# Optimization experiments

Hardware: AMD Instinct MI355X
Metric: run time of the kernel (lower is better)

Reference implementation:

```python
import jax, jax.numpy as jnp
import numpy as np

B, N, D = 4, 512, 256  # batch, num_diseases, feature_dim == hidden_dim
H = 256                # hidden_dim
EPS = 1e-5

def _layernorm(x, g, b):
    m = jnp.mean(x, axis=-1, keepdims=True)
    v = jnp.mean((x - m) ** 2, axis=-1, keepdims=True)
    return (x - m) * jax.lax.rsqrt(v + EPS) * g + b

def setup_inputs() -> dict:
    key = jax.random.key(0)
    ks = jax.random.split(key, 16)
    s = 0.02
    return {
        "x": jax.random.normal(ks[0], (B, N, D), jnp.float32),
        "area_matrix": jax.random.uniform(ks[1], (B, N), jnp.float32),
        "co_occurrence": jax.random.uniform(ks[2], (N, N), jnp.float32),
        "Wq": jax.random.normal(ks[3], (H, D), jnp.float32) * s,
        "bq": jnp.zeros((H,), jnp.float32),
        "Wk": jax.random.normal(ks[4], (H, D), jnp.float32) * s,
        "bk": jnp.zeros((H,), jnp.float32),
        "Wv": jax.random.normal(ks[5], (H, D), jnp.float32) * s,
        "bv": jnp.zeros((H,), jnp.float32),
        "We1": jax.random.normal(ks[6], (H, 2), jnp.float32) * 0.5,
        "be1": jnp.zeros((H,), jnp.float32),
        "We2": jax.random.normal(ks[7], (1, H), jnp.float32) * s,
        "be2": jnp.zeros((1,), jnp.float32),
        "Wo": jax.random.normal(ks[8], (H, H), jnp.float32) * s,
        "bo": jnp.zeros((H,), jnp.float32),
        "g_ot": jnp.ones((H,), jnp.float32),
        "b_ot": jnp.zeros((H,), jnp.float32),
        "g1": jnp.ones((H,), jnp.float32),
        "b1": jnp.zeros((H,), jnp.float32),
        "g2": jnp.ones((H,), jnp.float32),
        "b2": jnp.zeros((H,), jnp.float32),
    }

def reference(x, area_matrix, co_occurrence, Wq, bq, Wk, bk, Wv, bv,
              We1, be1, We2, be2, Wo, bo, g_ot, b_ot, g1, b1, g2, b2):
    # projections: (B, N, H)
    q = jnp.einsum('bnd,hd->bnh', x, Wq) + bq
    k = jnp.einsum('bnd,hd->bnh', x, Wk) + bk
    v = jnp.einsum('bnd,hd->bnh', x, Wv) + bv
    attn_scores = jnp.einsum('bih,bjh->bij', q, k) / jnp.sqrt(jnp.float32(H))
    # edge inputs: (B, N, N, 2) = stack(broadcast area along last N, broadcast co-occ along batch)
    area = jnp.broadcast_to(area_matrix[:, :, None], (B, N, N))
    co = jnp.broadcast_to(co_occurrence[None], (B, N, N))
    edge_inputs = jnp.stack([area, co], axis=-1)
    h = jax.nn.relu(jnp.einsum('bije,he->bijh', edge_inputs, We1) + be1)
    edge_weights = jax.nn.sigmoid(jnp.einsum('bijh,oh->bijo', h, We2) + be2)[..., 0]
    attn_probs = jax.nn.softmax(attn_scores * edge_weights, axis=-1)  # dropout = identity (eval)
    out = jnp.einsum('bij,bjh->bih', attn_probs, v)
    out = _layernorm(out, g1, b1)
    out = jax.nn.relu(_layernorm(jnp.einsum('bnh,oh->bno', out, Wo) + bo, g_ot, b_ot))
    out = _layernorm(out + x, g2, b2)
    return out
```

## Files before the change

### kernel.cpp

```cpp
#include <hip/hip_runtime.h>

typedef unsigned short u16;
typedef unsigned int u32;

#define NB 4
#define NN 512
#define ND 256
#define NH 256
#define TI 4

typedef __attribute__((ext_vector_type(8))) short short8;
typedef __attribute__((ext_vector_type(4))) float f32x4;

__device__ __forceinline__ u16 bfq(float f) {
    u32 t; __builtin_memcpy(&t, &f, 4);
    u32 r = (t + 0x7FFFu + ((t >> 16) & 1u)) >> 16;
    return (u16)r;
}

__device__ __forceinline__ short8 cvt8(float4 a, float4 b) {
    short8 r;
    r[0] = (short)bfq(a.x); r[1] = (short)bfq(a.y);
    r[2] = (short)bfq(a.z); r[3] = (short)bfq(a.w);
    r[4] = (short)bfq(b.x); r[5] = (short)bfq(b.y);
    r[6] = (short)bfq(b.z); r[7] = (short)bfq(b.w);
    return r;
}

__device__ __forceinline__ float waveReduceSum(float v) {
#pragma unroll
    for (int o = 32; o > 0; o >>= 1) v += __shfl_down(v, o);
    return v;
}

__device__ __forceinline__ void blockReduce8(float4& va, float4& vb, float4* red) {
#pragma unroll
    for (int o = 32; o > 0; o >>= 1) {
        va.x += __shfl_down(va.x, o); va.y += __shfl_down(va.y, o);
        va.z += __shfl_down(va.z, o); va.w += __shfl_down(va.w, o);
        vb.x += __shfl_down(vb.x, o); vb.y += __shfl_down(vb.y, o);
        vb.z += __shfl_down(vb.z, o); vb.w += __shfl_down(vb.w, o);
    }
    int wid = threadIdx.x >> 6;
    __syncthreads();
    if ((threadIdx.x & 63) == 0) { red[2 * wid] = va; red[2 * wid + 1] = vb; }
    __syncthreads();
    float4 ra = red[0], rb = red[1];
#pragma unroll
    for (int w = 1; w < 8; ++w) {
        float4 ua = red[2 * w], ub = red[2 * w + 1];
        ra.x += ua.x; ra.y += ua.y; ra.z += ua.z; ra.w += ua.w;
        rb.x += ub.x; rb.y += ub.y; rb.z += ub.z; rb.w += ub.w;
    }
    va = ra; vb = rb;
}

__global__ __launch_bounds__(256) void qkv_mfma(
    const float* __restrict__ x,
    const float* __restrict__ Wq, const float* __restrict__ bq,
    const float* __restrict__ Wk, const float* __restrict__ bk,
    const float* __restrict__ Wv, const float* __restrict__ bv,
    u16* __restrict__ qb, u16* __restrict__ kb, u16* __restrict__ vt)
{
    const int lane = threadIdx.x & 63, wave = threadIdx.x >> 6;
    const int r0 = blockIdx.x * 64 + wave * 16;
    const int out0 = blockIdx.y * 16;
    const int which = blockIdx.y >> 4;
    const float* W   = (which == 0) ? Wq : (which == 1) ? Wk : Wv;
    const float* bia = (which == 0) ? bq : (which == 1) ? bk : bv;

    const int m = lane & 15, koff = (lane >> 4) * 8;
    const float* Apf = x + (size_t)(r0 + m) * 256 + koff;
    const float* Bpf = W + (size_t)((out0 & 255) + m) * 256 + koff;

    f32x4 acc = {0.f, 0.f, 0.f, 0.f};
#pragma unroll
    for (int ks = 0; ks < 8; ++ks) {
        float4 a0 = *(const float4*)(Apf + ks * 32);
        float4 a1 = *(const float4*)(Apf + ks * 32 + 4);
        float4 b0 = *(const float4*)(Bpf + ks * 32);
        float4 b1 = *(const float4*)(Bpf + ks * 32 + 4);
        acc = __builtin_amdgcn_mfma_f32_16x16x32_bf16(cvt8(a0, a1), cvt8(b0, b1), acc, 0, 0, 0);
    }

    const int oc = (out0 + m) & 255;
    const float bias = bia[oc];
    const int rbase = r0 + (lane >> 4) * 4;
#pragma unroll
    for (int reg = 0; reg < 4; ++reg) {
        int R = rbase + reg;
        u16 val = bfq(acc[reg] + bias);
        if (which == 0)      qb[(size_t)R * 256 + oc] = val;
        else if (which == 1) kb[(size_t)R * 256 + oc] = val;
        else                 vt[((size_t)(R >> 9) * 256 + oc) * 512 + (R & 511)] = val;
    }
}

#define PSTR 520
#define YSTR 264
__global__ __launch_bounds__(512, 4) void fused_kernel(
    const float* __restrict__ x, const float* __restrict__ area, const float* __restrict__ co,
    const float* __restrict__ We1, const float* __restrict__ be1,
    const float* __restrict__ We2, const float* __restrict__ be2,
    const float* __restrict__ Wo, const float* __restrict__ bo,
    const float* __restrict__ g_ot, const float* __restrict__ b_ot,
    const float* __restrict__ g1, const float* __restrict__ b1,
    const float* __restrict__ g2, const float* __restrict__ b2,
    const u16* __restrict__ qb, const u16* __restrict__ kb,
    const u16* __restrict__ vt, float* __restrict__ out)
{
    const int tid = threadIdx.x;
    const int bsw = (blockIdx.x & 7) * 64 + (blockIdx.x >> 3);
    const int b = bsw >> 7;
    const int i0 = (bsw & 127) << 2;
    const int lane = tid & 63, w = tid >> 6;
    const int g = lane >> 4, c = lane & 15;
    const int hP = tid & 255, half = tid >> 8;

    __shared__ float histS[1024], histB[1024];
    __shared__ float pvbuf[1024];
    __shared__ u16 srow16[16 * PSTR];
    __shared__ u16 y16[16 * YSTR];
    __shared__ float4 red8b[16];
    __shared__ float sBaseS[4], sBaseB[4], redA[8], redB[8];

    const int m = lane & 15, koff = (lane >> 4) * 8;
    const u16* Ap    = qb + (size_t)(b * 512 + i0 + m) * 256 + koff;
    const u16* Kbase = kb + (size_t)(b * 512 + m) * 256 + koff;

    short8 afr[8];
#pragma unroll
    for (int ks = 0; ks < 8; ++ks) afr[ks] = *(const short8*)(Ap + ks * 32);

    float cov[4];
#pragma unroll
    for (int t = 0; t < 4; ++t)
        cov[t] = co[(size_t)(i0 + g) * NN + (w * 4 + t) * 16 + c];

    float xv[TI];
#pragma unroll
    for (int ti = 0; ti < TI; ++ti)
        xv[ti] = x[(size_t)(b * NN + i0 + ti) * ND + hP];

    const float bov  = bo[hP];
    const float g1v  = g1[hP],  b1v  = b1[hP];
    const float gotv = g_ot[hP], botv = b_ot[hP];
    const float g2v  = g2[hP],  b2v  = b2[hP];
    const float be2f = be2[0];

    histS[tid] = 0.f; histS[tid + 512] = 0.f;
    histB[tid] = 0.f; histB[tid + 512] = 0.f;
    {
        u32* s32 = (u32*)srow16;
        for (int i = tid; i < 4160; i += 512) s32[i] = 0u;
        u32* y32 = (u32*)y16;
        for (int i = tid; i < 2112; i += 512) y32[i] = 0u;
    }
    __syncthreads();

    {
        const int s = tid >> 7, h0 = tid & 127;
        const float a = area[b * NN + i0 + s];
        float baS = 0.f, baB = 0.f;
#pragma unroll
        for (int k = 0; k < 2; ++k) {
            const int h = h0 + 128 * k;
            const float w10 = We1[2 * h], w11 = We1[2 * h + 1];
            const float w2v = We2[h], be1v = be1[h];
            const float al = fmaf(a, w10, be1v);
            const float sl = w11 * w2v, bb = al * w2v;
            if (w11 == 0.f) {
                if (al > 0.f) baB += bb;
            } else {
                float tt = -al / w11;
                if (w11 > 0.f) {
                    if (tt <= 0.f)      { baS += sl; baB += bb; }
                    else if (tt < 1.f) {
                        int u = (int)(tt * 256.f); u = u > 255 ? 255 : u;
                        atomicAdd(&histS[s * 256 + u], sl);
                        atomicAdd(&histB[s * 256 + u], bb);
                    }
                } else {
                    if (tt >= 1.f)      { baS += sl; baB += bb; }
                    else if (tt > 0.f) {
                        baS += sl; baB += bb;
                        int u = (int)(tt * 256.f); u = u > 255 ? 255 : u;
                        atomicAdd(&histS[s * 256 + u], -sl);
                        atomicAdd(&histB[s * 256 + u], -bb);
                    }
                }
            }
        }
        float rS = waveReduceSum(baS), rB = waveReduceSum(baB);
        if (lane == 0) { redA[w] = rS; redB[w] = rB; }
    }

    f32x4 sacc[4];
    {
#pragma unroll
        for (int t = 0; t < 4; ++t) {
            const u16* Bp = Kbase + (size_t)(w * 4 + t) * 16 * 256;
            f32x4 acc = {0.f, 0.f, 0.f, 0.f};
#pragma unroll
            for (int ks = 0; ks < 8; ++ks) {
                short8 bb = *(const short8*)(Bp + ks * 32);
                acc = __builtin_amdgcn_mfma_f32_16x16x32_bf16(afr[ks], bb, acc, 0, 0, 0);
            }
            sacc[t] = acc;
        }
    }
    __syncthreads();
    if (tid < 4) {
        sBaseS[tid] = redA[2 * tid] + redA[2 * tid + 1];
        sBaseB[tid] = redB[2 * tid] + redB[2 * tid + 1];
    }

    {
        const int s = w & 3;
        float* hp = (w < 4) ? histS : histB;
        float b0 = hp[s * 256 + 4 * lane + 0];
        float b1 = hp[s * 256 + 4 * lane + 1];
        float b2 = hp[s * 256 + 4 * lane + 2];
        float b3 = hp[s * 256 + 4 * lane + 3];
        float p0 = b0, p1 = p0 + b1, p2 = p1 + b2, p3 = p2 + b3;
        float incl = p3;
#pragma unroll
        for (int off = 1; off < 64; off <<= 1) {
            float t = __shfl_up(incl, off);
            if (lane >= off) incl += t;
        }
        float excl = incl - p3;
        hp[s * 256 + 4 * lane + 0] = p0 + excl;
        hp[s * 256 + 4 * lane + 1] = p1 + excl;
        hp[s * 256 + 4 * lane + 2] = p2 + excl;
        hp[s * 256 + 4 * lane + 3] = p3 + excl;
    }
    __syncthreads();

    {
#pragma unroll
        for (int t = 0; t < 4; ++t) {
            const int j = (w * 4 + t) * 16 + c;
            float s0 = __shfl(sacc[t][0], c);
            float s1 = __shfl(sacc[t][1], c);
            float s2 = __shfl(sacc[t][2], c);
            float s3 = __shfl(sacc[t][3], c);
            float sv = (g == 0) ? s0 : (g == 1) ? s1 : (g == 2) ? s2 : s3;
            float cc = cov[t];
            int u = (int)(cc * 256.f); u = u > 255 ? 255 : u;
            float Sg = sBaseS[g] + histS[g * 256 + u];
            float Bg = sBaseB[g] + histB[g * 256 + u];
            float e = fmaf(cc, Sg, Bg) + be2f;
            float ew = 1.f / (1.f + __expf(-e));
            srow16[g * PSTR + j] = bfq(__expf(sv * 0.0625f * ew));
        }
    }
    __syncthreads();

    {
        const int t0 = 2 * w, t1 = 2 * w + 1;
        const u16* B0p = vt + ((size_t)(b * 256 + t0 * 16 + m)) * 512 + koff;
        const u16* B1p = vt + ((size_t)(b * 256 + t1 * 16 + m)) * 512 + koff;
        const u16* Arow = srow16 + m * PSTR + koff;
        f32x4 acc0 = {0.f, 0.f, 0.f, 0.f}, acc1 = {0.f, 0.f, 0.f, 0.f};
#pragma unroll
        for (int ks = 0; ks < 16; ++ks) {
            short8 a  = *(const short8*)(Arow + ks * 32);
            short8 b0 = *(const short8*)(B0p + ks * 32);
            short8 b1 = *(const short8*)(B1p + ks * 32);
            acc0 = __builtin_amdgcn_mfma_f32_16x16x32_bf16(a, b0, acc0, 0, 0, 0);
            acc1 = __builtin_amdgcn_mfma_f32_16x16x32_bf16(a, b1, acc1, 0, 0, 0);
        }
        if (lane < 16) {
#pragma unroll
            for (int reg = 0; reg < 4; ++reg) {
                pvbuf[reg * 256 + t0 * 16 + lane] = acc0[reg];
                pvbuf[reg * 256 + t1 * 16 + lane] = acc1[reg];
            }
        }
        __syncthreads();
    }

    float4 sa, sb;
    float accv[TI];
#pragma unroll
    for (int ti = 0; ti < TI; ++ti) {
        accv[ti] = (half == 0) ? pvbuf[ti * 256 + hP] : 0.f;
        ((float*)&sa)[ti] = accv[ti];
        ((float*)&sb)[ti] = accv[ti] * accv[ti];
    }
    blockReduce8(sa, sb, red8b);
    if (half == 0) {
#pragma unroll
        for (int ti = 0; ti < TI; ++ti) {
            float mean = ((const float*)&sa)[ti] * (1.f / 256.f);
            float var = fmaxf(((const float*)&sb)[ti] * (1.f / 256.f) - mean * mean, 0.f);
            y16[ti * YSTR + hP] = bfq((accv[ti] - mean) * rsqrtf(var + 1e-5f) * g1v + b1v);
        }
    }
    __syncthreads();

    {
        const int t0 = 2 * w, t1 = 2 * w + 1;
        const float* B0f = Wo + (size_t)(t0 * 16 + m) * 256 + koff;
        const float* B1f = Wo + (size_t)(t1 * 16 + m) * 256 + koff;
        const u16* Arow = y16 + m * YSTR + koff;
        f32x4 acc0 = {0.f, 0.f, 0.f, 0.f}, acc1 = {0.f, 0.f, 0.f, 0.f};
#pragma unroll
        for (int ks = 0; ks < 8; ++ks) {
            short8 a  = *(const short8*)(Arow + ks * 32);
            short8 b0 = cvt8(*(const float4*)(B0f + ks * 32), *(const float4*)(B0f + ks * 32 + 4));
            short8 b1 = cvt8(*(const float4*)(B1f + ks * 32), *(const float4*)(B1f + ks * 32 + 4));
            acc0 = __builtin_amdgcn_mfma_f32_16x16x32_bf16(a, b0, acc0, 0, 0, 0);
            acc1 = __builtin_amdgcn_mfma_f32_16x16x32_bf16(a, b1, acc1, 0, 0, 0);
        }
        if (lane < 16) {
#pragma unroll
            for (int reg = 0; reg < 4; ++reg) {
                pvbuf[reg * 256 + t0 * 16 + lane] = acc0[reg];
                pvbuf[reg * 256 + t1 * 16 + lane] = acc1[reg];
            }
        }
        __syncthreads();
    }

    float acc2[TI];
#pragma unroll
    for (int ti = 0; ti < TI; ++ti) {
        acc2[ti] = (half == 0) ? pvbuf[ti * 256 + hP] + bov : 0.f;
        ((float*)&sa)[ti] = acc2[ti];
        ((float*)&sb)[ti] = acc2[ti] * acc2[ti];
    }
    blockReduce8(sa, sb, red8b);
    float z[TI];
#pragma unroll
    for (int ti = 0; ti < TI; ++ti) {
        float mean = ((const float*)&sa)[ti] * (1.f / 256.f);
        float var = fmaxf(((const float*)&sb)[ti] * (1.f / 256.f) - mean * mean, 0.f);
        z[ti] = fmaxf((acc2[ti] - mean) * rsqrtf(var + 1e-5f) * gotv + botv, 0.f);
    }

    float tt[TI];
#pragma unroll
    for (int ti = 0; ti < TI; ++ti) {
        tt[ti] = (half == 0) ? z[ti] + xv[ti] : 0.f;
        ((float*)&sa)[ti] = tt[ti]; ((float*)&sb)[ti] = tt[ti] * tt[ti];
    }
    blockReduce8(sa, sb, red8b);
    if (half == 0) {
#pragma unroll
        for (int ti = 0; ti < TI; ++ti) {
            float mean = ((const float*)&sa)[ti] * (1.f / 256.f);
            float var = fmaxf(((const float*)&sb)[ti] * (1.f / 256.f) - mean * mean, 0.f);
            float o = (tt[ti] - mean) * rsqrtf(var + 1e-5f) * g2v + b2v;
            out[(size_t)(b * NN + i0 + ti) * NH + hP] = o;
        }
    }
}

extern "C" void kernel_launch(void* const* d_in, const int* in_sizes, int n_in,
                              void* d_out, int out_size, void* d_ws, size_t ws_size,
                              hipStream_t stream) {
    const float* x    = (const float*)d_in[0];
    const float* area = (const float*)d_in[1];
    const float* co   = (const float*)d_in[2];
    const float* Wq   = (const float*)d_in[3];
    const float* bq   = (const float*)d_in[4];
    const float* Wk   = (const float*)d_in[5];
    const float* bk   = (const float*)d_in[6];
    const float* Wv   = (const float*)d_in[7];
    const float* bv   = (const float*)d_in[8];
    const float* We1  = (const float*)d_in[9];
    const float* be1  = (const float*)d_in[10];
    const float* We2  = (const float*)d_in[11];
    const float* be2  = (const float*)d_in[12];
    const float* Wo   = (const float*)d_in[13];
    const float* bo   = (const float*)d_in[14];
    const float* g_ot = (const float*)d_in[15];
    const float* b_ot = (const float*)d_in[16];
    const float* g1   = (const float*)d_in[17];
    const float* b1   = (const float*)d_in[18];
    const float* g2   = (const float*)d_in[19];
    const float* b2   = (const float*)d_in[20];

    u16*  qb  = (u16*)d_ws;
    u16*  kb  = qb + (size_t)2048 * 256;
    u16*  vt  = kb + (size_t)2048 * 256;

    qkv_mfma<<<dim3(32, 48), 256, 0, stream>>>(x, Wq, bq, Wk, bk, Wv, bv, qb, kb, vt);
    fused_kernel<<<NB * NN / TI, 512, 0, stream>>>(x, area, co, We1, be1, We2, be2,
                                                   Wo, bo, g_ot, b_ot, g1, b1, g2, b2,
                                                   qb, kb, vt, (float*)d_out);
}
```

Before: 176.4 us.

## Halve rows per fused block, pre-convert Wo to bf16, stage QKV operands in LDS

The fused attention kernel now handles 2 query rows per block instead of 4, doubling the grid to 1024 blocks. The score, histogram and co-occurrence indexing are remapped so each wave's lanes cover two rows across paired column tiles. A new prep kernel converts Wo to bf16 once per call, so the fused kernel's output projection loads bf16 directly instead of converting fp32 in every block. The QKV projection now stages x and W tiles as bf16 in shared memory before the MFMA loop. The cost is an extra launch, and the 16-row MFMA tiles in the fused kernel now carry only 2 useful rows, so more K/V and Wo traffic is spent per output row.

```diff
diff --git a/kernel.cpp b/kernel.cpp
--- a/kernel.cpp
+++ b/kernel.cpp
@@ -7,7 +7,7 @@
 #define NN 512
 #define ND 256
 #define NH 256
-#define TI 4
+#define TI 2
 
 typedef __attribute__((ext_vector_type(8))) short short8;
 typedef __attribute__((ext_vector_type(4))) float f32x4;
@@ -16,15 +16,6 @@
     u32 t; __builtin_memcpy(&t, &f, 4);
     u32 r = (t + 0x7FFFu + ((t >> 16) & 1u)) >> 16;
     return (u16)r;
-}
-
-__device__ __forceinline__ short8 cvt8(float4 a, float4 b) {
-    short8 r;
-    r[0] = (short)bfq(a.x); r[1] = (short)bfq(a.y);
-    r[2] = (short)bfq(a.z); r[3] = (short)bfq(a.w);
-    r[4] = (short)bfq(b.x); r[5] = (short)bfq(b.y);
-    r[6] = (short)bfq(b.z); r[7] = (short)bfq(b.w);
-    return r;
 }
 
 __device__ __forceinline__ float waveReduceSum(float v) {
@@ -55,6 +46,7 @@
     va = ra; vb = rb;
 }
 
+#define XSTR 264
 __global__ __launch_bounds__(256) void qkv_mfma(
     const float* __restrict__ x,
     const float* __restrict__ Wq, const float* __restrict__ bq,
@@ -62,30 +54,53 @@
     const float* __restrict__ Wv, const float* __restrict__ bv,
     u16* __restrict__ qb, u16* __restrict__ kb, u16* __restrict__ vt)
 {
-    const int lane = threadIdx.x & 63, wave = threadIdx.x >> 6;
-    const int r0 = blockIdx.x * 64 + wave * 16;
+    const int tid = threadIdx.x;
+    const int lane = tid & 63, wave = tid >> 6;
+    const int which = blockIdx.y >> 4;
     const int out0 = blockIdx.y * 16;
-    const int which = blockIdx.y >> 4;
+    const int wr0 = (blockIdx.y & 15) * 16;
+    const int r0b = blockIdx.x * 64;
     const float* W   = (which == 0) ? Wq : (which == 1) ? Wk : Wv;
     const float* bia = (which == 0) ? bq : (which == 1) ? bk : bv;
 
+    __shared__ u16 xs[64 * XSTR];
+    __shared__ u16 ws[16 * XSTR];
+
+#pragma unroll
+    for (int i = 0; i < 16; ++i) {
+        const int f = i * 256 + tid;
+        const int row = f >> 6, col4 = f & 63;
+        float4 v = *(const float4*)(x + (size_t)(r0b + row) * 256 + col4 * 4);
+        u32 lo = (u32)bfq(v.x) | ((u32)bfq(v.y) << 16);
+        u32 hi = (u32)bfq(v.z) | ((u32)bfq(v.w) << 16);
+        *(uint2*)(xs + row * XSTR + col4 * 4) = make_uint2(lo, hi);
+    }
+#pragma unroll
+    for (int i = 0; i < 4; ++i) {
+        const int f = i * 256 + tid;
+        const int row = f >> 6, col4 = f & 63;
+        float4 v = *(const float4*)(W + (size_t)(wr0 + row) * 256 + col4 * 4);
+        u32 lo = (u32)bfq(v.x) | ((u32)bfq(v.y) << 16);
+        u32 hi = (u32)bfq(v.z) | ((u32)bfq(v.w) << 16);
+        *(uint2*)(ws + row * XSTR + col4 * 4) = make_uint2(lo, hi);
+    }
+    __syncthreads();
+
     const int m = lane & 15, koff = (lane >> 4) * 8;
-    const float* Apf = x + (size_t)(r0 + m) * 256 + koff;
-    const float* Bpf = W + (size_t)((out0 & 255) + m) * 256 + koff;
+    const u16* Ap = xs + (wave * 16 + m) * XSTR + koff;
+    const u16* Bp = ws + m * XSTR + koff;
 
     f32x4 acc = {0.f, 0.f, 0.f, 0.f};
 #pragma unroll
     for (int ks = 0; ks < 8; ++ks) {
-        float4 a0 = *(const float4*)(Apf + ks * 32);
-        float4 a1 = *(const float4*)(Apf + ks * 32 + 4);
-        float4 b0 = *(const float4*)(Bpf + ks * 32);
-        float4 b1 = *(const float4*)(Bpf + ks * 32 + 4);
-        acc = __builtin_amdgcn_mfma_f32_16x16x32_bf16(cvt8(a0, a1), cvt8(b0, b1), acc, 0, 0, 0);
+        short8 a  = *(const short8*)(Ap + ks * 32);
+        short8 bb = *(const short8*)(Bp + ks * 32);
+        acc = __builtin_amdgcn_mfma_f32_16x16x32_bf16(a, bb, acc, 0, 0, 0);
     }
 
     const int oc = (out0 + m) & 255;
     const float bias = bia[oc];
-    const int rbase = r0 + (lane >> 4) * 4;
+    const int rbase = r0b + wave * 16 + (lane >> 4) * 4;
 #pragma unroll
     for (int reg = 0; reg < 4; ++reg) {
         int R = rbase + reg;
@@ -102,27 +117,29 @@
     const float* __restrict__ x, const float* __restrict__ area, const float* __restrict__ co,
     const float* __restrict__ We1, const float* __restrict__ be1,
     const float* __restrict__ We2, const float* __restrict__ be2,
-    const float* __restrict__ Wo, const float* __restrict__ bo,
+    const u16* __restrict__ wob_dummy, const float* __restrict__ bo,
     const float* __restrict__ g_ot, const float* __restrict__ b_ot,
     const float* __restrict__ g1, const float* __restrict__ b1,
     const float* __restrict__ g2, const float* __restrict__ b2,
     const u16* __restrict__ qb, const u16* __restrict__ kb,
-    const u16* __restrict__ vt, float* __restrict__ out)
+    const u16* __restrict__ vt, const u16* __restrict__ wob,
+    float* __restrict__ out)
 {
     const int tid = threadIdx.x;
-    const int bsw = (blockIdx.x & 7) * 64 + (blockIdx.x >> 3);
-    const int b = bsw >> 7;
-    const int i0 = (bsw & 127) << 2;
+    const int bsw = (blockIdx.x & 7) * 128 + (blockIdx.x >> 3);
+    const int b = bsw >> 8;
+    const int i0 = (bsw & 255) << 1;
     const int lane = tid & 63, w = tid >> 6;
     const int g = lane >> 4, c = lane & 15;
+    const int r = g & 1, hsel = g >> 1;
     const int hP = tid & 255, half = tid >> 8;
 
-    __shared__ float histS[1024], histB[1024];
-    __shared__ float pvbuf[1024];
+    __shared__ float histS[512], histB[512];
+    __shared__ float pvbuf[512];
     __shared__ u16 srow16[16 * PSTR];
     __shared__ u16 y16[16 * YSTR];
     __shared__ float4 red8b[16];
-    __shared__ float sBaseS[4], sBaseB[4], redA[8], redB[8];
+    __shared__ float sBaseS[2], sBaseB[2], redA[8], redB[8];
 
     const int m = lane & 15, koff = (lane >> 4) * 8;
     const u16* Ap    = qb + (size_t)(b * 512 + i0 + m) * 256 + koff;
@@ -132,10 +149,10 @@
 #pragma unroll
     for (int ks = 0; ks < 8; ++ks) afr[ks] = *(const short8*)(Ap + ks * 32);
 
-    float cov[4];
-#pragma unroll
-    for (int t = 0; t < 4; ++t)
-        cov[t] = co[(size_t)(i0 + g) * NN + (w * 4 + t) * 16 + c];
+    float cov[2];
+#pragma unroll
+    for (int t = 0; t < 2; ++t)
+        cov[t] = co[(size_t)(i0 + r) * NN + (w * 4 + 2 * t + hsel) * 16 + c];
 
     float xv[TI];
 #pragma unroll
@@ -148,8 +165,7 @@
     const float g2v  = g2[hP],  b2v  = b2[hP];
     const float be2f = be2[0];
 
-    histS[tid] = 0.f; histS[tid + 512] = 0.f;
-    histB[tid] = 0.f; histB[tid + 512] = 0.f;
+    histS[tid & 511] = 0.f; histB[tid & 511] = 0.f;
     {
         u32* s32 = (u32*)srow16;
         for (int i = tid; i < 4160; i += 512) s32[i] = 0u;
@@ -159,12 +175,10 @@
     __syncthreads();
 
     {
-        const int s = tid >> 7, h0 = tid & 127;
+        const int s = tid >> 8, h = tid & 255;
         const float a = area[b * NN + i0 + s];
         float baS = 0.f, baB = 0.f;
-#pragma unroll
-        for (int k = 0; k < 2; ++k) {
-            const int h = h0 + 128 * k;
+        {
             const float w10 = We1[2 * h], w11 = We1[2 * h + 1];
             const float w2v = We2[h], be1v = be1[h];
             const float al = fmaf(a, w10, be1v);
@@ -210,49 +224,53 @@
         }
     }
     __syncthreads();
-    if (tid < 4) {
-        sBaseS[tid] = redA[2 * tid] + redA[2 * tid + 1];
-        sBaseB[tid] = redB[2 * tid] + redB[2 * tid + 1];
+    if (tid < 2) {
+        sBaseS[tid] = redA[4 * tid] + redA[4 * tid + 1] + redA[4 * tid + 2] + redA[4 * tid + 3];
+        sBaseB[tid] = redB[4 * tid] + redB[4 * tid + 1] + redB[4 * tid + 2] + redB[4 * tid + 3];
     }
 
     {
         const int s = w & 3;
-        float* hp = (w < 4) ? histS : histB;
-        float b0 = hp[s * 256 + 4 * lane + 0];
-        float b1 = hp[s * 256 + 4 * lane + 1];
-        float b2 = hp[s * 256 + 4 * lane + 2];
-        float b3 = hp[s * 256 + 4 * lane + 3];
-        float p0 = b0, p1 = p0 + b1, p2 = p1 + b2, p3 = p2 + b3;
-        float incl = p3;
-#pragma unroll
-        for (int off = 1; off < 64; off <<= 1) {
-            float t = __shfl_up(incl, off);
-            if (lane >= off) incl += t;
-        }
-        float excl = incl - p3;
-        hp[s * 256 + 4 * lane + 0] = p0 + excl;
-        hp[s * 256 + 4 * lane + 1] = p1 + excl;
-        hp[s * 256 + 4 * lane + 2] = p2 + excl;
-        hp[s * 256 + 4 * lane + 3] = p3 + excl;
-    }
-    __syncthreads();
-
-    {
-#pragma unroll
-        for (int t = 0; t < 4; ++t) {
-            const int j = (w * 4 + t) * 16 + c;
-            float s0 = __shfl(sacc[t][0], c);
-            float s1 = __shfl(sacc[t][1], c);
-            float s2 = __shfl(sacc[t][2], c);
-            float s3 = __shfl(sacc[t][3], c);
-            float sv = (g == 0) ? s0 : (g == 1) ? s1 : (g == 2) ? s2 : s3;
+        if (s < 2) {
+            float* hp = (w < 4) ? histS : histB;
+            float b0 = hp[s * 256 + 4 * lane + 0];
+            float b1 = hp[s * 256 + 4 * lane + 1];
+            float b2 = hp[s * 256 + 4 * lane + 2];
+            float b3 = hp[s * 256 + 4 * lane + 3];
+            float p0 = b0, p1 = p0 + b1, p2 = p1 + b2, p3 = p2 + b3;
+            float incl = p3;
+#pragma unroll
+            for (int off = 1; off < 64; off <<= 1) {
+                float t = __shfl_up(incl, off);
+                if (lane >= off) incl += t;
+            }
+            float excl = incl - p3;
+            hp[s * 256 + 4 * lane + 0] = p0 + excl;
+            hp[s * 256 + 4 * lane + 1] = p1 + excl;
+            hp[s * 256 + 4 * lane + 2] = p2 + excl;
+            hp[s * 256 + 4 * lane + 3] = p3 + excl;
+        }
+    }
+    __syncthreads();
+
+    {
+#pragma unroll
+        for (int t = 0; t < 2; ++t) {
+            const int te = 2 * t, to = 2 * t + 1;
+            float e0 = __shfl(sacc[te][0], c);
+            float e1 = __shfl(sacc[te][1], c);
+            float o0 = __shfl(sacc[to][0], c);
+            float o1 = __shfl(sacc[to][1], c);
+            float sv = hsel ? (r ? o1 : o0) : (r ? e1 : e0);
+            const int tt = te + hsel;
+            const int j = (w * 4 + tt) * 16 + c;
             float cc = cov[t];
             int u = (int)(cc * 256.f); u = u > 255 ? 255 : u;
-            float Sg = sBaseS[g] + histS[g * 256 + u];
-            float Bg = sBaseB[g] + histB[g * 256 + u];
+            float Sg = sBaseS[r] + histS[r * 256 + u];
+            float Bg = sBaseB[r] + histB[r * 256 + u];
             float e = fmaf(cc, Sg, Bg) + be2f;
             float ew = 1.f / (1.f + __expf(-e));
-            srow16[g * PSTR + j] = bfq(__expf(sv * 0.0625f * ew));
+            srow16[r * PSTR + j] = bfq(__expf(sv * 0.0625f * ew));
         }
     }
     __syncthreads();
@@ -273,7 +291,7 @@
         }
         if (lane < 16) {
 #pragma unroll
-            for (int reg = 0; reg < 4; ++reg) {
+            for (int reg = 0; reg < TI; ++reg) {
                 pvbuf[reg * 256 + t0 * 16 + lane] = acc0[reg];
                 pvbuf[reg * 256 + t1 * 16 + lane] = acc1[reg];
             }
@@ -281,7 +299,7 @@
         __syncthreads();
     }
 
-    float4 sa, sb;
+    float4 sa = {0.f, 0.f, 0.f, 0.f}, sb = {0.f, 0.f, 0.f, 0.f};
     float accv[TI];
 #pragma unroll
     for (int ti = 0; ti < TI; ++ti) {
@@ -302,21 +320,21 @@
 
     {
         const int t0 = 2 * w, t1 = 2 * w + 1;
-        const float* B0f = Wo + (size_t)(t0 * 16 + m) * 256 + koff;
-        const float* B1f = Wo + (size_t)(t1 * 16 + m) * 256 + koff;
+        const u16* B0p = wob + (size_t)(t0 * 16 + m) * 256 + koff;
+        const u16* B1p = wob + (size_t)(t1 * 16 + m) * 256 + koff;
         const u16* Arow = y16 + m * YSTR + koff;
         f32x4 acc0 = {0.f, 0.f, 0.f, 0.f}, acc1 = {0.f, 0.f, 0.f, 0.f};
 #pragma unroll
         for (int ks = 0; ks < 8; ++ks) {
             short8 a  = *(const short8*)(Arow + ks * 32);
-            short8 b0 = cvt8(*(const float4*)(B0f + ks * 32), *(const float4*)(B0f + ks * 32 + 4));
-            short8 b1 = cvt8(*(const float4*)(B1f + ks * 32), *(const float4*)(B1f + ks * 32 + 4));
+            short8 b0 = *(const short8*)(B0p + ks * 32);
+            short8 b1 = *(const short8*)(B1p + ks * 32);
             acc0 = __builtin_amdgcn_mfma_f32_16x16x32_bf16(a, b0, acc0, 0, 0, 0);
             acc1 = __builtin_amdgcn_mfma_f32_16x16x32_bf16(a, b1, acc1, 0, 0, 0);
         }
         if (lane < 16) {
 #pragma unroll
-            for (int reg = 0; reg < 4; ++reg) {
+            for (int reg = 0; reg < TI; ++reg) {
                 pvbuf[reg * 256 + t0 * 16 + lane] = acc0[reg];
                 pvbuf[reg * 256 + t1 * 16 + lane] = acc1[reg];
             }
@@ -340,11 +358,11 @@
         z[ti] = fmaxf((acc2[ti] - mean) * rsqrtf(var + 1e-5f) * gotv + botv, 0.f);
     }
 
-    float tt[TI];
+    float tt2[TI];
 #pragma unroll
     for (int ti = 0; ti < TI; ++ti) {
-        tt[ti] = (half == 0) ? z[ti] + xv[ti] : 0.f;
-        ((float*)&sa)[ti] = tt[ti]; ((float*)&sb)[ti] = tt[ti] * tt[ti];
+        tt2[ti] = (half == 0) ? z[ti] + xv[ti] : 0.f;
+        ((float*)&sa)[ti] = tt2[ti]; ((float*)&sb)[ti] = tt2[ti] * tt2[ti];
     }
     blockReduce8(sa, sb, red8b);
     if (half == 0) {
@@ -352,10 +370,19 @@
         for (int ti = 0; ti < TI; ++ti) {
             float mean = ((const float*)&sa)[ti] * (1.f / 256.f);
             float var = fmaxf(((const float*)&sb)[ti] * (1.f / 256.f) - mean * mean, 0.f);
-            float o = (tt[ti] - mean) * rsqrtf(var + 1e-5f) * g2v + b2v;
+            float o = (tt2[ti] - mean) * rsqrtf(var + 1e-5f) * g2v + b2v;
             out[(size_t)(b * NN + i0 + ti) * NH + hP] = o;
         }
     }
+}
+
+__global__ __launch_bounds__(256) void wo_prep(const float* __restrict__ Wo, u16* __restrict__ wob)
+{
+    const int idx4 = (blockIdx.x * 256 + threadIdx.x) * 4;
+    float4 f = *(const float4*)(Wo + idx4);
+    u32 lo = (u32)bfq(f.x) | ((u32)bfq(f.y) << 16);
+    u32 hi = (u32)bfq(f.z) | ((u32)bfq(f.w) << 16);
+    *(uint2*)(wob + idx4) = make_uint2(lo, hi);
 }
 
 extern "C" void kernel_launch(void* const* d_in, const int* in_sizes, int n_in,
@@ -386,9 +413,12 @@
     u16*  qb  = (u16*)d_ws;
     u16*  kb  = qb + (size_t)2048 * 256;
     u16*  vt  = kb + (size_t)2048 * 256;
-
+    u16*  wob = vt + (size_t)2048 * 256;
+
+    wo_prep<<<64, 256, 0, stream>>>(Wo, wob);
     qkv_mfma<<<dim3(32, 48), 256, 0, stream>>>(x, Wq, bq, Wk, bk, Wv, bv, qb, kb, vt);
     fused_kernel<<<NB * NN / TI, 512, 0, stream>>>(x, area, co, We1, be1, We2, be2,
-                                                   Wo, bo, g_ot, b_ot, g1, b1, g2, b2,
-                                                   qb, kb, vt, (float*)d_out);
-}
+                                                   (const u16*)nullptr, bo,
+                                                   g_ot, b_ot, g1, b1, g2, b2,
+                                                   qb, kb, vt, wob, (float*)d_out);
+}
```

After: 198.4 us. 12.5% more time.
